# Kernel tuning notes

Hardware: AMD Instinct MI355X
Metric: run time of the kernel (lower is better)

Reference implementation:

```python
import jax, jax.numpy as jnp
import numpy as np

N_NODES = 100000
N_EDGES = 3200000
D_IN = 96      # sum(latent_dim)
D_OUT = 32     # latent_dim[-1]
N_HEADS = 4
LEAKY_SLOPE = 0.2


def setup_inputs() -> dict:
    key = jax.random.key(0)
    k_x, k_w, k_a, k_src, k_dst = jax.random.split(key, 5)
    x = jax.random.normal(k_x, (N_NODES, D_IN), dtype=jnp.float32)
    # per-head GAT params (xavier-ish scale)
    W = jax.random.normal(k_w, (N_HEADS, D_IN, D_OUT), dtype=jnp.float32) * (1.414 / np.sqrt(D_IN))
    a = jax.random.normal(k_a, (N_HEADS, 2 * D_OUT), dtype=jnp.float32) * 0.1
    edge_src = jax.random.randint(k_src, (N_EDGES,), 0, N_NODES)
    edge_dst = jax.random.randint(k_dst, (N_EDGES,), 0, N_NODES)
    return {"x": x, "W": W, "a": a, "edge_src": edge_src, "edge_dst": edge_dst}


def reference(x, W, a, edge_src, edge_dst):
    # Multi-head sparse GAT layer (SpGraphAttentionLayer, concat=True, eval mode).
    N = x.shape[0]
    n_heads, _, d_out = W.shape
    outs = []
    for i in range(n_heads):  # small fixed head loop; data dims fully vectorized
        h = x @ W[i]                                   # [N, d_out]
        # a @ cat(h[src], h[dst]) == h[src]@a1 + h[dst]@a2 (avoids [E, 2*d_out] concat)
        s = h[edge_src] @ a[i, :d_out] + h[edge_dst] @ a[i, d_out:]   # [E]
        edge_e = jnp.exp(-jax.nn.leaky_relu(s, LEAKY_SLOPE))          # [E]
        # sparse_coo(edge, edge_e, [N,N]) @ h  ==  scatter-add of edge_e * h[dst] into src
        msg = edge_e[:, None] * h[edge_dst]                           # [E, d_out]
        h_prime = jax.ops.segment_sum(msg, edge_src, num_segments=N)  # [N, d_out]
        outs.append(jax.nn.elu(h_prime))
    return jnp.concatenate(outs, axis=1)  # [N, n_heads * d_out]
```

## Files before the change

### kernel.cpp

```cpp
#include <hip/hip_runtime.h>
#include <hip/hip_bf16.h>

#define DIN 96
#define DOUT 32
#define NH 4
#define DTOT 128
#define SLOPE 0.2f
#define NPBF 64
#define BSH 7
#define BNODES 128
#define MAXB 1024
#define EPB 4096
#define BCAP 5632

__device__ __forceinline__ unsigned int packbf2(float lo, float hi) {
    unsigned int a = __float_as_uint(lo), b = __float_as_uint(hi);
    a += 0x7fffu + ((a >> 16) & 1u);
    b += 0x7fffu + ((b >> 16) & 1u);
    return (a >> 16) | (b & 0xffff0000u);
}

__global__ __launch_bounds__(256) void prep_kernel(
    const float* __restrict__ x, const float* __restrict__ W,
    const float* __restrict__ a,
    const int* __restrict__ esrc, const int* __restrict__ edst,
    unsigned int* __restrict__ hq,
    float2* __restrict__ usrc, float2* __restrict__ vdst,
    int* __restrict__ gcur0, unsigned int* __restrict__ binned,
    int n_nodes, int n_edges, int nb, int sblocks, int fblocks)
{
    __shared__ float Wlo[DIN * 64];
    __shared__ float Whi[DIN * 64];
    __shared__ float al[NH * 2 * DOUT];
    const int t = threadIdx.x;
    const int bid = (int)blockIdx.x;
    const int q3 = bid / 3;
    const int r3 = bid - q3 * 3;

    if (r3 == 0 && q3 < sblocks) {
        int* bc = (int*)Wlo;
        for (int i = t; i < nb; i += 256) bc[i] = 0;
        __syncthreads();

        const int base = q3 * EPB;
        const int end = min(base + EPB, n_edges);
        const bool full = (end - base) == EPB;

        int se[16], de[16];
        if (full) {
            const int4* s4p = (const int4*)(esrc + base);
            const int4* d4p = (const int4*)(edst + base);
#pragma unroll
            for (int j = 0; j < 4; ++j) {
                int4 s4 = s4p[j * 256 + t];
                int4 d4 = d4p[j * 256 + t];
                se[j * 4 + 0] = s4.x; se[j * 4 + 1] = s4.y;
                se[j * 4 + 2] = s4.z; se[j * 4 + 3] = s4.w;
                de[j * 4 + 0] = d4.x; de[j * 4 + 1] = d4.y;
                de[j * 4 + 2] = d4.z; de[j * 4 + 3] = d4.w;
            }
#pragma unroll
            for (int j = 0; j < 16; ++j)
                atomicAdd(&bc[se[j] >> BSH], 1);
        } else {
#pragma unroll
            for (int j = 0; j < 16; ++j) {
                const int e = base + j * 256 + t;
                se[j] = (e < end) ? esrc[e] : 0;
                de[j] = (e < end) ? edst[e] : 0;
                if (e < end) atomicAdd(&bc[se[j] >> BSH], 1);
            }
        }
        __syncthreads();

        for (int i = t; i < nb; i += 256) {
            int c = bc[i];
            bc[i] = (c > 0) ? (i * BCAP + atomicAdd(&gcur0[i], c)) : 0;
        }
        __syncthreads();

        if (full) {
#pragma unroll
            for (int j = 0; j < 16; ++j) {
                int s = se[j];
                int pos = atomicAdd(&bc[s >> BSH], 1);
                binned[pos] = ((unsigned int)(s & (BNODES - 1)) << 17) | (unsigned int)de[j];
            }
        } else {
#pragma unroll
            for (int j = 0; j < 16; ++j) {
                const int e = base + j * 256 + t;
                if (e < end) {
                    int s = se[j];
                    int pos = atomicAdd(&bc[s >> BSH], 1);
                    binned[pos] = ((unsigned int)(s & (BNODES - 1)) << 17) | (unsigned int)de[j];
                }
            }
        }
        return;
    }

    const int fid = bid - min(q3 + (r3 ? 1 : 0), sblocks);
    if (fid >= fblocks) return;

    for (int i = t; i < DIN * DTOT; i += 256) {
        int k = i >> 7, c = i & 127;
        int head = c >> 5, j = c & 31;
        float w = W[head * (DIN * DOUT) + k * DOUT + j];
        int cbi = c >> 3, jj = c & 7;
        if (jj < 4) Wlo[(k << 6) + (cbi << 2) + jj] = w;
        else        Whi[(k << 6) + (cbi << 2) + (jj - 4)] = w;
    }
    for (int i = t; i < NH * 2 * DOUT; i += 256) al[i] = a[i];
    __syncthreads();

    const int cbi = t & 15;
    const int ng = t >> 4;
    const int node0 = fid * NPBF;
    const int g0 = node0 + ng * 4;

    bool ok[4];
    const float* xp[4];
#pragma unroll
    for (int i = 0; i < 4; ++i) {
        ok[i] = (g0 + i) < n_nodes;
        xp[i] = x + (size_t)(g0 + i) * DIN;
    }

    float acc[4][8];
#pragma unroll
    for (int i = 0; i < 4; ++i)
#pragma unroll
        for (int j = 0; j < 8; ++j) acc[i][j] = 0.f;

    for (int k = 0; k < DIN; k += 4) {
        float4 xv[4];
#pragma unroll
        for (int i = 0; i < 4; ++i)
            xv[i] = ok[i] ? *(const float4*)(xp[i] + k)
                          : make_float4(0.f, 0.f, 0.f, 0.f);
#pragma unroll
        for (int kk = 0; kk < 4; ++kk) {
            const float4 wlo = *(const float4*)&Wlo[((k + kk) << 6) + (cbi << 2)];
            const float4 whi = *(const float4*)&Whi[((k + kk) << 6) + (cbi << 2)];
#pragma unroll
            for (int i = 0; i < 4; ++i) {
                const float xvv = (kk == 0) ? xv[i].x : (kk == 1) ? xv[i].y
                                 : (kk == 2) ? xv[i].z : xv[i].w;
                acc[i][0] = fmaf(xvv, wlo.x, acc[i][0]);
                acc[i][1] = fmaf(xvv, wlo.y, acc[i][1]);
                acc[i][2] = fmaf(xvv, wlo.z, acc[i][2]);
                acc[i][3] = fmaf(xvv, wlo.w, acc[i][3]);
                acc[i][4] = fmaf(xvv, whi.x, acc[i][4]);
                acc[i][5] = fmaf(xvv, whi.y, acc[i][5]);
                acc[i][6] = fmaf(xvv, whi.z, acc[i][6]);
                acc[i][7] = fmaf(xvv, whi.w, acc[i][7]);
            }
        }
    }

    const int head = cbi >> 2;
    const int j0 = (cbi & 3) << 3;
#pragma unroll
    for (int i = 0; i < 4; ++i) {
        float ps = 0.f, pd = 0.f;
#pragma unroll
        for (int j = 0; j < 8; ++j) {
            ps += acc[i][j] * al[head * 64 + j0 + j];
            pd += acc[i][j] * al[head * 64 + 32 + j0 + j];
        }
        ps += __shfl_xor(ps, 1); ps += __shfl_xor(ps, 2);
        pd += __shfl_xor(pd, 1); pd += __shfl_xor(pd, 2);
        const int g = g0 + i;
        if (ok[i]) {
            uint4 pk;
            pk.x = packbf2(acc[i][0], acc[i][1]);
            pk.y = packbf2(acc[i][2], acc[i][3]);
            pk.z = packbf2(acc[i][4], acc[i][5]);
            pk.w = packbf2(acc[i][6], acc[i][7]);
            *(uint4*)&hq[(size_t)g * 64 + (cbi << 2)] = pk;
            if ((cbi & 3) == 0) {
                usrc[g * NH + head] = make_float2(__expf(-ps), __expf(-SLOPE * ps));
                vdst[g * NH + head] = make_float2(__expf(-pd), __expf(-SLOPE * pd));
            }
        }
    }
}

__global__ __launch_bounds__(512) void bucket_kernel(
    const int* __restrict__ gcur0,
    const unsigned int* __restrict__ binned,
    const unsigned int* __restrict__ hv,
    const float2* __restrict__ usrc, const float2* __restrict__ vdst,
    float* __restrict__ out, int n_nodes)
{
    __shared__ int slist[BCAP];
    __shared__ int dcnt[BNODES];
    __shared__ int sc[BNODES];
    __shared__ int dcur[BNODES];
    const int t = threadIdx.x;
    const int b = (int)blockIdx.x;
    const unsigned base = (unsigned)b * BCAP;
    int cnt = gcur0[b];
    if (cnt > BCAP - 512) cnt = BCAP - 512;
    const int node0 = b << BSH;

    if (t < BNODES) dcnt[t] = 0;
    __syncthreads();
    for (int i = t; i < cnt; i += 512)
        atomicAdd(&dcnt[binned[base + i] >> 17], 1);
    __syncthreads();
    int pd = 0;
    if (t < BNODES) { pd = (dcnt[t] + 3) & ~3; sc[t] = pd; }
    __syncthreads();
    for (int off = 1; off < BNODES; off <<= 1) {
        int v = 0;
        if (t < BNODES && t >= off) v = sc[t - off];
        __syncthreads();
        if (t < BNODES) sc[t] += v;
        __syncthreads();
    }
    if (t < BNODES) dcur[t] = sc[t] - pd;
    __syncthreads();
    for (int i = t; i < cnt; i += 512) {
        unsigned int w = binned[base + i];
        int pos = atomicAdd(&dcur[w >> 17], 1);
        slist[pos] = (int)(w & 0x1ffffu);
    }
    __syncthreads();

    const int l = t & 63;
    const int head = l >> 4;
    const unsigned loff = (unsigned)l << 2;
    const unsigned hoff = (unsigned)head << 3;
    const char* __restrict__ hvb = (const char*)hv;
    const char* __restrict__ vdb = (const char*)vdst;
    const int sub = t >> 6;

#define LDV(c) (*(const float2*)(vdb + ((((unsigned)(c)) << 5) + hoff)))
#define LDW(c) (*(const unsigned int*)(hvb + ((((unsigned)(c)) << 8) + loff)))
#define COMP(vv, ww, AX, AY) do {                                   \
        float e_ = fminf(u.x * (vv).x, u.y * (vv).y);               \
        AX = fmaf(e_, __uint_as_float((ww) << 16), AX);             \
        AY = fmaf(e_, __uint_as_float((ww) & 0xffff0000u), AY);     \
    } while (0)

    for (int q = 0; q < BNODES / 8; ++q) {
        const int nd = q * 8 + sub;
        const int node = node0 + nd;
        if (node >= n_nodes) break;
        const int d = dcnt[nd];
        const int beg = dcur[nd] - d;
        const float2 u = usrc[(unsigned)node * 4u + head];

        float ax0 = 0.f, ay0 = 0.f, ax1 = 0.f, ay1 = 0.f;
        float ax2 = 0.f, ay2 = 0.f, ax3 = 0.f, ay3 = 0.f;
        int k = 0;
        if (d >= 4) {
            int4 cA = *(const int4*)&slist[beg];
            float2 vA0 = LDV(cA.x), vA1 = LDV(cA.y), vA2 = LDV(cA.z), vA3 = LDV(cA.w);
            unsigned wA0 = LDW(cA.x), wA1 = LDW(cA.y), wA2 = LDW(cA.z), wA3 = LDW(cA.w);

            for (; k + 12 <= d; k += 8) {
                int4 cB = *(const int4*)&slist[beg + k + 4];
                float2 vB0 = LDV(cB.x), vB1 = LDV(cB.y), vB2 = LDV(cB.z), vB3 = LDV(cB.w);
                unsigned wB0 = LDW(cB.x), wB1 = LDW(cB.y), wB2 = LDW(cB.z), wB3 = LDW(cB.w);
                COMP(vA0, wA0, ax0, ay0); COMP(vA1, wA1, ax1, ay1);
                COMP(vA2, wA2, ax2, ay2); COMP(vA3, wA3, ax3, ay3);
                int4 cN = *(const int4*)&slist[beg + k + 8];
                vA0 = LDV(cN.x); vA1 = LDV(cN.y); vA2 = LDV(cN.z); vA3 = LDV(cN.w);
                wA0 = LDW(cN.x); wA1 = LDW(cN.y); wA2 = LDW(cN.z); wA3 = LDW(cN.w);
                COMP(vB0, wB0, ax0, ay0); COMP(vB1, wB1, ax1, ay1);
                COMP(vB2, wB2, ax2, ay2); COMP(vB3, wB3, ax3, ay3);
            }
            if (k + 8 <= d) {
                int4 cB = *(const int4*)&slist[beg + k + 4];
                float2 vB0 = LDV(cB.x), vB1 = LDV(cB.y), vB2 = LDV(cB.z), vB3 = LDV(cB.w);
                unsigned wB0 = LDW(cB.x), wB1 = LDW(cB.y), wB2 = LDW(cB.z), wB3 = LDW(cB.w);
                COMP(vA0, wA0, ax0, ay0); COMP(vA1, wA1, ax1, ay1);
                COMP(vA2, wA2, ax2, ay2); COMP(vA3, wA3, ax3, ay3);
                COMP(vB0, wB0, ax0, ay0); COMP(vB1, wB1, ax1, ay1);
                COMP(vB2, wB2, ax2, ay2); COMP(vB3, wB3, ax3, ay3);
                k += 8;
            } else {
                COMP(vA0, wA0, ax0, ay0); COMP(vA1, wA1, ax1, ay1);
                COMP(vA2, wA2, ax2, ay2); COMP(vA3, wA3, ax3, ay3);
                k += 4;
            }
        }
        for (; k < d; ++k) {
            int c = slist[beg + k];
            float2 v = LDV(c);
            unsigned w = LDW(c);
            COMP(v, w, ax0, ay0);
        }
        float rx = (ax0 + ax1) + (ax2 + ax3);
        float ry = (ay0 + ay1) + (ay2 + ay3);
        rx = rx > 0.f ? rx : __expf(rx) - 1.f;
        ry = ry > 0.f ? ry : __expf(ry) - 1.f;
        ((float2*)out)[(unsigned)node * 64u + l] = make_float2(rx, ry);
    }
#undef LDV
#undef LDW
#undef COMP
}

extern "C" void kernel_launch(void* const* d_in, const int* in_sizes, int n_in,
                              void* d_out, int out_size, void* d_ws, size_t ws_size,
                              hipStream_t stream)
{
    const float* x  = (const float*)d_in[0];
    const float* W  = (const float*)d_in[1];
    const float* a  = (const float*)d_in[2];
    const int* esrc = (const int*)d_in[3];
    const int* edst = (const int*)d_in[4];
    const int n_nodes = in_sizes[0] / DIN;
    const int n_edges = in_sizes[3];
    float* out = (float*)d_out;

    const int nb = (n_nodes + BNODES - 1) >> BSH;

    unsigned int* hq = (unsigned int*)d_ws;
    float2* usrc = (float2*)(hq + (size_t)n_nodes * 64);
    float2* vdst = usrc + (size_t)n_nodes * NH;
    int* gcur0  = (int*)(vdst + (size_t)n_nodes * NH);
    unsigned int* binned = (unsigned int*)(gcur0 + MAXB);

    hipMemsetAsync(gcur0, 0, MAXB * sizeof(int), stream);

    const int SB = (n_edges + EPB - 1) / EPB;
    const int FB = (n_nodes + NPBF - 1) / NPBF;
    int grid = SB + FB;
    if (grid < 3 * SB - 2) grid = 3 * SB - 2;

    prep_kernel<<<grid, 256, 0, stream>>>(
        x, W, a, esrc, edst, hq, usrc, vdst, gcur0, binned,
        n_nodes, n_edges, nb, SB, FB);

    bucket_kernel<<<nb, 512, 0, stream>>>(
        gcur0, binned, hq, usrc, vdst, out, n_nodes);
}
```

Baseline: 418.7 us.

## Split bucket processing into four sub-blocks per bin and separate prep kernels

The bucket kernel now launches four blocks per 128-node bin. Each block scans the whole bin's edge list, keeps only the edges whose source falls in its 32-node quarter, and stages them in shared memory before the local counting sort. The combined prep kernel is split into separate feature-transform and bin-scatter kernels launched back to back, so the two no longer overlap. The aim is more parallelism and smaller shared-memory footprints in the bucket stage. In exchange, every block rereads the full bin (four times the binned reads), there is one more kernel launch, and the fixed QSL cap silently drops edges if a quarter holds more than 2304.

```diff
diff --git a/kernel.cpp b/kernel.cpp
--- a/kernel.cpp
+++ b/kernel.cpp
@@ -12,6 +12,8 @@
 #define MAXB 1024
 #define EPB 4096
 #define BCAP 5632
+#define QSL  2304
+#define SLSZ 2432
 
 __device__ __forceinline__ unsigned int packbf2(float lo, float hi) {
     unsigned int a = __float_as_uint(lo), b = __float_as_uint(hi);
@@ -20,88 +22,17 @@
     return (a >> 16) | (b & 0xffff0000u);
 }
 
-__global__ __launch_bounds__(256) void prep_kernel(
+__global__ __launch_bounds__(256) void feat_kernel(
     const float* __restrict__ x, const float* __restrict__ W,
     const float* __restrict__ a,
-    const int* __restrict__ esrc, const int* __restrict__ edst,
     unsigned int* __restrict__ hq,
     float2* __restrict__ usrc, float2* __restrict__ vdst,
-    int* __restrict__ gcur0, unsigned int* __restrict__ binned,
-    int n_nodes, int n_edges, int nb, int sblocks, int fblocks)
+    int n_nodes)
 {
     __shared__ float Wlo[DIN * 64];
     __shared__ float Whi[DIN * 64];
     __shared__ float al[NH * 2 * DOUT];
     const int t = threadIdx.x;
-    const int bid = (int)blockIdx.x;
-    const int q3 = bid / 3;
-    const int r3 = bid - q3 * 3;
-
-    if (r3 == 0 && q3 < sblocks) {
-        int* bc = (int*)Wlo;
-        for (int i = t; i < nb; i += 256) bc[i] = 0;
-        __syncthreads();
-
-        const int base = q3 * EPB;
-        const int end = min(base + EPB, n_edges);
-        const bool full = (end - base) == EPB;
-
-        int se[16], de[16];
-        if (full) {
-            const int4* s4p = (const int4*)(esrc + base);
-            const int4* d4p = (const int4*)(edst + base);
-#pragma unroll
-            for (int j = 0; j < 4; ++j) {
-                int4 s4 = s4p[j * 256 + t];
-                int4 d4 = d4p[j * 256 + t];
-                se[j * 4 + 0] = s4.x; se[j * 4 + 1] = s4.y;
-                se[j * 4 + 2] = s4.z; se[j * 4 + 3] = s4.w;
-                de[j * 4 + 0] = d4.x; de[j * 4 + 1] = d4.y;
-                de[j * 4 + 2] = d4.z; de[j * 4 + 3] = d4.w;
-            }
-#pragma unroll
-            for (int j = 0; j < 16; ++j)
-                atomicAdd(&bc[se[j] >> BSH], 1);
-        } else {
-#pragma unroll
-            for (int j = 0; j < 16; ++j) {
-                const int e = base + j * 256 + t;
-                se[j] = (e < end) ? esrc[e] : 0;
-                de[j] = (e < end) ? edst[e] : 0;
-                if (e < end) atomicAdd(&bc[se[j] >> BSH], 1);
-            }
-        }
-        __syncthreads();
-
-        for (int i = t; i < nb; i += 256) {
-            int c = bc[i];
-            bc[i] = (c > 0) ? (i * BCAP + atomicAdd(&gcur0[i], c)) : 0;
-        }
-        __syncthreads();
-
-        if (full) {
-#pragma unroll
-            for (int j = 0; j < 16; ++j) {
-                int s = se[j];
-                int pos = atomicAdd(&bc[s >> BSH], 1);
-                binned[pos] = ((unsigned int)(s & (BNODES - 1)) << 17) | (unsigned int)de[j];
-            }
-        } else {
-#pragma unroll
-            for (int j = 0; j < 16; ++j) {
-                const int e = base + j * 256 + t;
-                if (e < end) {
-                    int s = se[j];
-                    int pos = atomicAdd(&bc[s >> BSH], 1);
-                    binned[pos] = ((unsigned int)(s & (BNODES - 1)) << 17) | (unsigned int)de[j];
-                }
-            }
-        }
-        return;
-    }
-
-    const int fid = bid - min(q3 + (r3 ? 1 : 0), sblocks);
-    if (fid >= fblocks) return;
 
     for (int i = t; i < DIN * DTOT; i += 256) {
         int k = i >> 7, c = i & 127;
@@ -116,7 +47,7 @@
 
     const int cbi = t & 15;
     const int ng = t >> 4;
-    const int node0 = fid * NPBF;
+    const int node0 = blockIdx.x * NPBF;
     const int g0 = node0 + ng * 4;
 
     bool ok[4];
@@ -187,6 +118,73 @@
     }
 }
 
+__global__ __launch_bounds__(256) void binscatter_kernel(
+    const int* __restrict__ esrc, const int* __restrict__ edst,
+    int* __restrict__ gcur0, unsigned int* __restrict__ binned,
+    int n_edges, int nb)
+{
+    __shared__ int bc[MAXB];
+    const int t = threadIdx.x;
+    for (int i = t; i < nb; i += 256) bc[i] = 0;
+    __syncthreads();
+
+    const int base = blockIdx.x * EPB;
+    const int end = min(base + EPB, n_edges);
+    const bool full = (end - base) == EPB;
+
+    int se[16], de[16];
+    if (full) {
+        const int4* s4p = (const int4*)(esrc + base);
+        const int4* d4p = (const int4*)(edst + base);
+#pragma unroll
+        for (int j = 0; j < 4; ++j) {
+            int4 s4 = s4p[j * 256 + t];
+            int4 d4 = d4p[j * 256 + t];
+            se[j * 4 + 0] = s4.x; se[j * 4 + 1] = s4.y;
+            se[j * 4 + 2] = s4.z; se[j * 4 + 3] = s4.w;
+            de[j * 4 + 0] = d4.x; de[j * 4 + 1] = d4.y;
+            de[j * 4 + 2] = d4.z; de[j * 4 + 3] = d4.w;
+        }
+#pragma unroll
+        for (int j = 0; j < 16; ++j)
+            atomicAdd(&bc[se[j] >> BSH], 1);
+    } else {
+#pragma unroll
+        for (int j = 0; j < 16; ++j) {
+            const int e = base + j * 256 + t;
+            se[j] = (e < end) ? esrc[e] : 0;
+            de[j] = (e < end) ? edst[e] : 0;
+            if (e < end) atomicAdd(&bc[se[j] >> BSH], 1);
+        }
+    }
+    __syncthreads();
+
+    for (int i = t; i < nb; i += 256) {
+        int c = bc[i];
+        bc[i] = (c > 0) ? (i * BCAP + atomicAdd(&gcur0[i], c)) : 0;
+    }
+    __syncthreads();
+
+    if (full) {
+#pragma unroll
+        for (int j = 0; j < 16; ++j) {
+            int s = se[j];
+            int pos = atomicAdd(&bc[s >> BSH], 1);
+            binned[pos] = ((unsigned int)(s & (BNODES - 1)) << 17) | (unsigned int)de[j];
+        }
+    } else {
+#pragma unroll
+        for (int j = 0; j < 16; ++j) {
+            const int e = base + j * 256 + t;
+            if (e < end) {
+                int s = se[j];
+                int pos = atomicAdd(&bc[s >> BSH], 1);
+                binned[pos] = ((unsigned int)(s & (BNODES - 1)) << 17) | (unsigned int)de[j];
+            }
+        }
+    }
+}
+
 __global__ __launch_bounds__(512) void bucket_kernel(
     const int* __restrict__ gcur0,
     const unsigned int* __restrict__ binned,
@@ -194,37 +192,53 @@
     const float2* __restrict__ usrc, const float2* __restrict__ vdst,
     float* __restrict__ out, int n_nodes)
 {
-    __shared__ int slist[BCAP];
-    __shared__ int dcnt[BNODES];
-    __shared__ int sc[BNODES];
-    __shared__ int dcur[BNODES];
+    __shared__ unsigned int wbuf[QSL];
+    __shared__ __align__(16) int slist[SLSZ];
+    __shared__ int dcnt[32];
+    __shared__ int sc[32];
+    __shared__ int dcur[32];
+    __shared__ int qn_s;
     const int t = threadIdx.x;
-    const int b = (int)blockIdx.x;
-    const unsigned base = (unsigned)b * BCAP;
-    int cnt = gcur0[b];
+    const int p = (int)blockIdx.x >> 2;
+    const int q = (int)blockIdx.x & 3;
+    const unsigned pbase = (unsigned)p * BCAP;
+    int cnt = gcur0[p];
     if (cnt > BCAP - 512) cnt = BCAP - 512;
-    const int node0 = b << BSH;
-
-    if (t < BNODES) dcnt[t] = 0;
-    __syncthreads();
-    for (int i = t; i < cnt; i += 512)
-        atomicAdd(&dcnt[binned[base + i] >> 17], 1);
-    __syncthreads();
+    const int node0 = (p << BSH) + (q << 5);
+
+    if (t < 32) dcnt[t] = 0;
+    if (t == 0) qn_s = 0;
+    __syncthreads();
+
+    for (int i = t; i < cnt; i += 512) {
+        unsigned int w = binned[pbase + i];
+        int s = (int)(w >> 17);
+        if ((s >> 5) == q) {
+            int pos = atomicAdd(&qn_s, 1);
+            if (pos < QSL) {
+                wbuf[pos] = w;
+                atomicAdd(&dcnt[s & 31], 1);
+            }
+        }
+    }
+    __syncthreads();
+    int qn = qn_s; if (qn > QSL) qn = QSL;
+
     int pd = 0;
-    if (t < BNODES) { pd = (dcnt[t] + 3) & ~3; sc[t] = pd; }
-    __syncthreads();
-    for (int off = 1; off < BNODES; off <<= 1) {
+    if (t < 32) { pd = (dcnt[t] + 3) & ~3; sc[t] = pd; }
+    __syncthreads();
+    for (int off = 1; off < 32; off <<= 1) {
         int v = 0;
-        if (t < BNODES && t >= off) v = sc[t - off];
+        if (t < 32 && t >= off) v = sc[t - off];
         __syncthreads();
-        if (t < BNODES) sc[t] += v;
+        if (t < 32) sc[t] += v;
         __syncthreads();
     }
-    if (t < BNODES) dcur[t] = sc[t] - pd;
-    __syncthreads();
-    for (int i = t; i < cnt; i += 512) {
-        unsigned int w = binned[base + i];
-        int pos = atomicAdd(&dcur[w >> 17], 1);
+    if (t < 32) dcur[t] = sc[t] - pd;
+    __syncthreads();
+    for (int i = t; i < qn; i += 512) {
+        unsigned int w = wbuf[i];
+        int pos = atomicAdd(&dcur[(w >> 17) & 31], 1);
         slist[pos] = (int)(w & 0x1ffffu);
     }
     __syncthreads();
@@ -245,8 +259,8 @@
         AY = fmaf(e_, __uint_as_float((ww) & 0xffff0000u), AY);     \
     } while (0)
 
-    for (int q = 0; q < BNODES / 8; ++q) {
-        const int nd = q * 8 + sub;
+    for (int r = 0; r < 4; ++r) {
+        const int nd = r * 8 + sub;
         const int node = node0 + nd;
         if (node >= n_nodes) break;
         const int d = dcnt[nd];
@@ -328,15 +342,12 @@
 
     hipMemsetAsync(gcur0, 0, MAXB * sizeof(int), stream);
 
-    const int SB = (n_edges + EPB - 1) / EPB;
-    const int FB = (n_nodes + NPBF - 1) / NPBF;
-    int grid = SB + FB;
-    if (grid < 3 * SB - 2) grid = 3 * SB - 2;
-
-    prep_kernel<<<grid, 256, 0, stream>>>(
-        x, W, a, esrc, edst, hq, usrc, vdst, gcur0, binned,
-        n_nodes, n_edges, nb, SB, FB);
-
-    bucket_kernel<<<nb, 512, 0, stream>>>(
+    feat_kernel<<<(n_nodes + NPBF - 1) / NPBF, 256, 0, stream>>>(
+        x, W, a, hq, usrc, vdst, n_nodes);
+
+    binscatter_kernel<<<(n_edges + EPB - 1) / EPB, 256, 0, stream>>>(
+        esrc, edst, gcur0, binned, n_edges, nb);
+
+    bucket_kernel<<<nb * 4, 512, 0, stream>>>(
         gcur0, binned, hq, usrc, vdst, out, n_nodes);
 }
```

Result: no change. 413.1 us (-1.3%).
